# Performance work log

Measured on AMD Instinct MI355X. Metric: run time of the kernel, lower is better.

The kernel has to match this reference:

```python
import jax, jax.numpy as jnp
import numpy as np

EPS = 1e-12

def _l2_normalize(v, axis):
    norm = jnp.linalg.norm(v, ord=2, axis=axis, keepdims=True)
    return v / jnp.maximum(norm, EPS)

def setup_inputs() -> dict:
    key = jax.random.key(0)
    k1, k2, k3 = jax.random.split(key, 3)
    B, H, W, D, K = 16, 56, 56, 512, 32
    x = jax.random.normal(k1, (B, H, W, D), dtype=jnp.float32)
    # 1x1 conv weight (no bias): equivalent to a (D,K) matmul; he_normal-ish scale
    Wc = jax.random.normal(k2, (D, K), dtype=jnp.float32) * jnp.sqrt(2.0 / D)
    # cluster centers, original shape (1,1,1,512,32) -> stored as (D,K)
    C = jax.random.normal(k3, (D, K), dtype=jnp.float32) * jnp.sqrt(2.0 / D)
    return {"x": x, "Wc": Wc, "C": C}

def reference(x, Wc, C):
    # soft-assignment: 1x1 conv + softmax over clusters
    s = jnp.einsum('bhwd,dk->bhwk', x, Wc)          # (B,H,W,K)
    a = jax.nn.softmax(s, axis=-1)                   # (B,H,W,K)
    # v[b,d,k] = sum_{h,w} a[b,h,w,k] * (x[b,h,w,d] + C[d,k])
    #          = einsum(a,x) + C * sum_{h,w} a   (avoids (B,H,W,D,K) intermediate)
    ax = jnp.einsum('bhwk,bhwd->bdk', a, x)          # (B,D,K)
    a_sum = jnp.sum(a, axis=(1, 2))                  # (B,K)
    v = ax + C[None, :, :] * a_sum[:, None, :]       # (B,D,K)
    # intra-normalize over cluster axis (dim=2), flatten, L2 normalize
    v = _l2_normalize(v, axis=2)
    v = v.reshape(v.shape[0], -1)                    # (B, D*K)
    return _l2_normalize(v, axis=1)
```

## Files before the change

kernel.cpp:

```cpp
#include <hip/hip_runtime.h>
#include <math.h>


#define BATCH 16
#define HW    3136
#define DIM   512
#define KCL   32
#define NCHK  49
#define SLABF (BATCH * DIM * KCL + 256)

typedef __attribute__((ext_vector_type(8))) short short8;
typedef __attribute__((ext_vector_type(4))) float f32x4;

__device__ __forceinline__ void atomAddF(float* p, float v) {
    unsafeAtomicAdd(p, v);
}

__device__ __forceinline__ unsigned short f2bf(float f) {
    unsigned u = __float_as_uint(f);
    return (unsigned short)((u + 0x7FFFu + ((u >> 16) & 1u)) >> 16);
}

#define XS_STR  136
#define WTC_STR 136
#define AT_STR  72
#define XT_STR  72

#define LOAD_PX(PX, DC)                                                        \
    _Pragma("unroll")                                                          \
    for (int i = 0; i < 8; ++i) {                                              \
        int f = i * 256 + t;                                                   \
        PX[i] = *(const float4*)(x + ((size_t)(n0 + (f >> 5)) * DIM + (DC) + (f & 31) * 4)); \
    }

#define LOAD_WC(WC, DC)                                                        \
    _Pragma("unroll")                                                          \
    for (int i = 0; i < 4; ++i) {                                              \
        int f = i * 256 + t;                                                   \
        WC[i] = *(const float4*)(Wc + (size_t)((DC) + (f >> 3)) * KCL + (f & 7) * 4); \
    }

#define P1_STAGE(PX, WC)                                                       \
    __syncthreads();                                                           \
    _Pragma("unroll")                                                          \
    for (int i = 0; i < 8; ++i) {                                              \
        int f = i * 256 + t;                                                   \
        ushort4 w;                                                             \
        w.x = f2bf(PX[i].x); w.y = f2bf(PX[i].y);                              \
        w.z = f2bf(PX[i].z); w.w = f2bf(PX[i].w);                              \
        *(ushort4*)&xs[(f >> 5) * XS_STR + (f & 31) * 4] = w;                  \
    }                                                                          \
    _Pragma("unroll")                                                          \
    for (int i = 0; i < 4; ++i) {                                              \
        int f  = i * 256 + t;                                                  \
        int d  = f >> 3;                                                       \
        int k4 = (f & 7) * 4;                                                  \
        wt[(k4 + 0) * WTC_STR + d] = f2bf(WC[i].x);                            \
        wt[(k4 + 1) * WTC_STR + d] = f2bf(WC[i].y);                            \
        wt[(k4 + 2) * WTC_STR + d] = f2bf(WC[i].z);                            \
        wt[(k4 + 3) * WTC_STR + d] = f2bf(WC[i].w);                            \
    }                                                                          \
    __syncthreads();

#define P1_MFMA()                                                              \
    _Pragma("unroll")                                                          \
    for (int ds_ = 0; ds_ < 4; ++ds_) {                                        \
        const int dloc = ds_ * 32 + quad * 8;                                  \
        short8 af = *(const short8*)&xs[(wv * 16 + l15) * XS_STR + dloc];      \
        short8 b0 = *(const short8*)&wt[l15 * WTC_STR + dloc];                 \
        short8 b1 = *(const short8*)&wt[(16 + l15) * WTC_STR + dloc];          \
        acc0 = __builtin_amdgcn_mfma_f32_16x16x32_bf16(af, b0, acc0, 0, 0, 0); \
        acc1 = __builtin_amdgcn_mfma_f32_16x16x32_bf16(af, b1, acc1, 0, 0, 0); \
    }

#define LOAD_PF(PF, DC)                                                        \
    _Pragma("unroll")                                                          \
    for (int i = 0; i < 8; ++i) {                                              \
        const int p = (pg0 + 2 * i) * 4;                                       \
        _Pragma("unroll")                                                      \
        for (int j = 0; j < 4; ++j)                                            \
            PF[i * 4 + j] = xb[(size_t)(p + j) * DIM + (DC)];                  \
    }

#define P2_STAGE(PF)                                                           \
    __syncthreads();                                                           \
    _Pragma("unroll")                                                          \
    for (int i = 0; i < 8; ++i) {                                              \
        const int p = (pg0 + 2 * i) * 4;                                       \
        ushort4 w;                                                             \
        w.x = f2bf(PF[i * 4 + 0]); w.y = f2bf(PF[i * 4 + 1]);                  \
        w.z = f2bf(PF[i * 4 + 2]); w.w = f2bf(PF[i * 4 + 3]);                  \
        *(ushort4*)&xs[dl * XT_STR + (p ^ (((dl >> 3) & 7) << 3))] = w;        \
    }                                                                          \
    __syncthreads();

#define P2_MFMA_STORE(DC)                                                      \
    {                                                                          \
        f32x4 z = {0.f, 0.f, 0.f, 0.f};                                        \
        f32x4 pacc[2][2];                                                      \
        pacc[0][0] = z; pacc[0][1] = z; pacc[1][0] = z; pacc[1][1] = z;        \
        _Pragma("unroll")                                                      \
        for (int s_ = 0; s_ < 2; ++s_) {                                       \
            const int pb = s_ * 32 + quad * 8;                                 \
            short8 bf0 = *(const short8*)&aT[l15 * AT_STR + pb];               \
            short8 bf1 = *(const short8*)&aT[(16 + l15) * AT_STR + pb];        \
            _Pragma("unroll")                                                  \
            for (int m2 = 0; m2 < 2; ++m2) {                                   \
                const int dloc = (wv * 2 + m2) * 16 + l15;                     \
                short8 af = *(const short8*)&xs[dloc * XT_STR + (pb ^ (((dloc >> 3) & 7) << 3))]; \
                pacc[m2][0] = __builtin_amdgcn_mfma_f32_16x16x32_bf16(af, bf0, pacc[m2][0], 0, 0, 0); \
                pacc[m2][1] = __builtin_amdgcn_mfma_f32_16x16x32_bf16(af, bf1, pacc[m2][1], 0, 0, 0); \
            }                                                                  \
        }                                                                      \
        _Pragma("unroll")                                                      \
        for (int m2 = 0; m2 < 2; ++m2) {                                       \
            const int dr = (DC) + (wv * 2 + m2) * 16 + quad * 4;               \
            _Pragma("unroll")                                                  \
            for (int r = 0; r < 4; ++r) {                                      \
                vp[(size_t)(dr + r) * KCL + l15]      = pacc[m2][0][r];        \
                vp[(size_t)(dr + r) * KCL + 16 + l15] = pacc[m2][1][r];        \
            }                                                                  \
        }                                                                      \
    }

__global__ __launch_bounds__(256, 3) void k_sax(const float* __restrict__ x,
                                                const float* __restrict__ Wc,
                                                float* __restrict__ vpart,
                                                float* __restrict__ a_sum) {
    __shared__ unsigned short xs[9216];
    __shared__ unsigned short wt[32 * WTC_STR];
    __shared__ unsigned short aT[KCL * AT_STR];
    __shared__ float asum_l[4][32];
    const int t    = threadIdx.x;
    const int lane = t & 63;
    const int wv   = t >> 6;
    const int l15  = lane & 15;
    const int quad = lane >> 4;
    const int n0   = blockIdx.x * 64;
    const int b    = n0 / HW;
    const int ch   = blockIdx.x % NCHK;

    f32x4 acc0 = {0.f, 0.f, 0.f, 0.f};
    f32x4 acc1 = {0.f, 0.f, 0.f, 0.f};

    float4 pxA[8], pxB[8], wcA[4], wcB[4];
    LOAD_PX(pxA, 0);    LOAD_WC(wcA, 0);
    LOAD_PX(pxB, 128);  LOAD_WC(wcB, 128);

    P1_STAGE(pxA, wcA);
    LOAD_PX(pxA, 256);  LOAD_WC(wcA, 256);
    P1_MFMA();
    P1_STAGE(pxB, wcB);
    LOAD_PX(pxB, 384);  LOAD_WC(wcB, 384);
    P1_MFMA();
    P1_STAGE(pxA, wcA);
    P1_MFMA();
    P1_STAGE(pxB, wcB);
    P1_MFMA();

    float at0 = 0.f, at1 = 0.f;
#pragma unroll
    for (int r = 0; r < 4; ++r) {
        float m = fmaxf(acc0[r], acc1[r]);
        m = fmaxf(m, __shfl_xor(m, 1));
        m = fmaxf(m, __shfl_xor(m, 2));
        m = fmaxf(m, __shfl_xor(m, 4));
        m = fmaxf(m, __shfl_xor(m, 8));
        float e0 = __expf(acc0[r] - m);
        float e1 = __expf(acc1[r] - m);
        float s = e0 + e1;
        s += __shfl_xor(s, 1);
        s += __shfl_xor(s, 2);
        s += __shfl_xor(s, 4);
        s += __shfl_xor(s, 8);
        float inv = 1.f / s;
        float a0 = e0 * inv, a1 = e1 * inv;
        const int pos = wv * 16 + quad * 4 + r;
        aT[l15 * AT_STR + pos]        = f2bf(a0);
        aT[(16 + l15) * AT_STR + pos] = f2bf(a1);
        at0 += a0; at1 += a1;
    }
    at0 += __shfl_xor(at0, 16); at0 += __shfl_xor(at0, 32);
    at1 += __shfl_xor(at1, 16); at1 += __shfl_xor(at1, 32);
    if (quad == 0) {
        asum_l[wv][l15]      = at0;
        asum_l[wv][16 + l15] = at1;
    }

    const int dl  = t & 127;
    const int pg0 = t >> 7;
    const float* xb = x + (size_t)n0 * DIM + dl;
    float* vp = vpart + (size_t)ch * SLABF + (size_t)b * DIM * KCL;

    float pfA[32], pfB[32];
    LOAD_PF(pfA, 0);
    LOAD_PF(pfB, 128);

    __syncthreads();
    if (t < 32)
        atomAddF(&a_sum[b * KCL + t],
                 asum_l[0][t] + asum_l[1][t] + asum_l[2][t] + asum_l[3][t]);

    P2_STAGE(pfA);
    LOAD_PF(pfA, 256);
    P2_MFMA_STORE(0);
    P2_STAGE(pfB);
    LOAD_PF(pfB, 384);
    P2_MFMA_STORE(128);
    P2_STAGE(pfA);
    P2_MFMA_STORE(256);
    P2_STAGE(pfB);
    P2_MFMA_STORE(384);
}

__global__ __launch_bounds__(256) void k_norm1(const float* __restrict__ vpart,
                                               const float* __restrict__ a_sum,
                                               const float* __restrict__ Cc,
                                               float* __restrict__ out,
                                               float* __restrict__ ssq) {
    const int t = threadIdx.x;
    const int row = blockIdx.x * 8 + (t >> 5);
    const int k = t & 31;
    const int b = row >> 9;
    const int d = row & 511;

    const float* vp = vpart + (size_t)row * KCL + k;
    float s0 = 0.f, s1 = 0.f, s2 = 0.f, s3 = 0.f;
#pragma unroll
    for (int ps = 0; ps < 48; ps += 4) {
        s0 += vp[(size_t)(ps + 0) * SLABF];
        s1 += vp[(size_t)(ps + 1) * SLABF];
        s2 += vp[(size_t)(ps + 2) * SLABF];
        s3 += vp[(size_t)(ps + 3) * SLABF];
    }
    s0 += vp[(size_t)48 * SLABF];
    float v = (s0 + s1) + (s2 + s3) + Cc[d * KCL + k] * a_sum[b * KCL + k];

    float ss = v * v;
    ss += __shfl_xor(ss, 1, 32);  ss += __shfl_xor(ss, 2, 32);
    ss += __shfl_xor(ss, 4, 32);  ss += __shfl_xor(ss, 8, 32);
    ss += __shfl_xor(ss, 16, 32);
    float inv = 1.f / fmaxf(sqrtf(ss), 1e-12f);
    float r = v * inv;
    out[(size_t)row * KCL + k] = r;

    float bs = r * r;
    for (int off = 32; off > 0; off >>= 1) bs += __shfl_down(bs, off, 64);
    __shared__ float red[4];
    if ((t & 63) == 0) red[t >> 6] = bs;
    __syncthreads();
    if (t == 0) atomAddF(&ssq[b], (red[0] + red[1]) + (red[2] + red[3]));
}

__global__ __launch_bounds__(256) void k_norm2(float* __restrict__ out,
                                               const float* __restrict__ ssq) {
    const int i4 = blockIdx.x * 256 + threadIdx.x;
    const int b = i4 >> 12;
    float inv = 1.f / fmaxf(sqrtf(ssq[b]), 1e-12f);
    float4 v = *(float4*)(out + (size_t)i4 * 4);
    v.x *= inv; v.y *= inv; v.z *= inv; v.w *= inv;
    *(float4*)(out + (size_t)i4 * 4) = v;
}

extern "C" void kernel_launch(void* const* d_in, const int* in_sizes, int n_in,
                              void* d_out, int out_size, void* d_ws, size_t ws_size,
                              hipStream_t stream) {
    const float* x  = (const float*)d_in[0];
    const float* Wc = (const float*)d_in[1];
    const float* Cc = (const float*)d_in[2];
    float* out = (float*)d_out;

    char* ws = (char*)d_ws;
    float* vpart = (float*)ws;
    float* a_sum = (float*)(ws + (size_t)NCHK * SLABF * 4);
    float* ssq   = (float*)(ws + (size_t)NCHK * SLABF * 4 + 2048);

    hipMemsetAsync(a_sum, 0, 2048 + 64, stream);

    k_sax  <<<784, 256, 0, stream>>>(x, Wc, vpart, a_sum);
    k_norm1<<<1024, 256, 0, stream>>>(vpart, a_sum, Cc, out, ssq);
    k_norm2<<<256, 256, 0, stream>>>(out, ssq);
}
```

Baseline: 195.1 us.

## Load phase-1 x fragments directly into registers and stage full Wc once in LDS

Phase 1 of the fused soft-assign kernel no longer stages x tiles through shared memory. Each lane loads its MFMA A-fragment straight from global memory with double-buffered float4 prefetch and converts it to bf16 in registers. The whole Wc matrix is transposed into LDS once at kernel start, and that buffer is reused for the phase-2 x tile. Phase 2 gives each wave its own 32 rows and drops the barrier before each staging step, which removes several barriers and LDS round trips. The risks are higher register pressure and uncoalesced strided row loads, plus possible hazards from the removed barriers.

Result: no change. 198.2 us (+1.6%).

```diff
diff --git a/kernel.cpp b/kernel.cpp
--- a/kernel.cpp
+++ b/kernel.cpp
@@ -21,78 +21,35 @@
     return (unsigned short)((u + 0x7FFFu + ((u >> 16) & 1u)) >> 16);
 }
 
-#define XS_STR  136
-#define WTC_STR 136
-#define AT_STR  72
-#define XT_STR  72
-
-#define LOAD_PX(PX, DC)                                                        \
-    _Pragma("unroll")                                                          \
-    for (int i = 0; i < 8; ++i) {                                              \
-        int f = i * 256 + t;                                                   \
-        PX[i] = *(const float4*)(x + ((size_t)(n0 + (f >> 5)) * DIM + (DC) + (f & 31) * 4)); \
-    }
-
-#define LOAD_WC(WC, DC)                                                        \
-    _Pragma("unroll")                                                          \
-    for (int i = 0; i < 4; ++i) {                                              \
-        int f = i * 256 + t;                                                   \
-        WC[i] = *(const float4*)(Wc + (size_t)((DC) + (f >> 3)) * KCL + (f & 7) * 4); \
-    }
-
-#define P1_STAGE(PX, WC)                                                       \
-    __syncthreads();                                                           \
-    _Pragma("unroll")                                                          \
-    for (int i = 0; i < 8; ++i) {                                              \
-        int f = i * 256 + t;                                                   \
-        ushort4 w;                                                             \
-        w.x = f2bf(PX[i].x); w.y = f2bf(PX[i].y);                              \
-        w.z = f2bf(PX[i].z); w.w = f2bf(PX[i].w);                              \
-        *(ushort4*)&xs[(f >> 5) * XS_STR + (f & 31) * 4] = w;                  \
-    }                                                                          \
-    _Pragma("unroll")                                                          \
-    for (int i = 0; i < 4; ++i) {                                              \
-        int f  = i * 256 + t;                                                  \
-        int d  = f >> 3;                                                       \
-        int k4 = (f & 7) * 4;                                                  \
-        wt[(k4 + 0) * WTC_STR + d] = f2bf(WC[i].x);                            \
-        wt[(k4 + 1) * WTC_STR + d] = f2bf(WC[i].y);                            \
-        wt[(k4 + 2) * WTC_STR + d] = f2bf(WC[i].z);                            \
-        wt[(k4 + 3) * WTC_STR + d] = f2bf(WC[i].w);                            \
-    }                                                                          \
-    __syncthreads();
-
-#define P1_MFMA()                                                              \
-    _Pragma("unroll")                                                          \
-    for (int ds_ = 0; ds_ < 4; ++ds_) {                                        \
-        const int dloc = ds_ * 32 + quad * 8;                                  \
-        short8 af = *(const short8*)&xs[(wv * 16 + l15) * XS_STR + dloc];      \
-        short8 b0 = *(const short8*)&wt[l15 * WTC_STR + dloc];                 \
-        short8 b1 = *(const short8*)&wt[(16 + l15) * WTC_STR + dloc];          \
-        acc0 = __builtin_amdgcn_mfma_f32_16x16x32_bf16(af, b0, acc0, 0, 0, 0); \
-        acc1 = __builtin_amdgcn_mfma_f32_16x16x32_bf16(af, b1, acc1, 0, 0, 0); \
-    }
+__device__ __forceinline__ short8 pack_frag(float4 lo, float4 hi) {
+    union { unsigned short h[8]; short8 s; } r;
+    r.h[0] = f2bf(lo.x); r.h[1] = f2bf(lo.y); r.h[2] = f2bf(lo.z); r.h[3] = f2bf(lo.w);
+    r.h[4] = f2bf(hi.x); r.h[5] = f2bf(hi.y); r.h[6] = f2bf(hi.z); r.h[7] = f2bf(hi.w);
+    return r.s;
+}
+
+#define WT_STR 520
+#define AT_STR 72
+#define XT_STR 72
 
 #define LOAD_PF(PF, DC)                                                        \
     _Pragma("unroll")                                                          \
     for (int i = 0; i < 8; ++i) {                                              \
-        const int p = (pg0 + 2 * i) * 4;                                       \
+        const int p = (ph + 2 * i) * 4;                                        \
         _Pragma("unroll")                                                      \
         for (int j = 0; j < 4; ++j)                                            \
-            PF[i * 4 + j] = xb[(size_t)(p + j) * DIM + (DC)];                  \
+            PF[i * 4 + j] = xc[(size_t)(p + j) * DIM + (DC)];                  \
     }
 
 #define P2_STAGE(PF)                                                           \
-    __syncthreads();                                                           \
     _Pragma("unroll")                                                          \
     for (int i = 0; i < 8; ++i) {                                              \
-        const int p = (pg0 + 2 * i) * 4;                                       \
+        const int p = (ph + 2 * i) * 4;                                        \
         ushort4 w;                                                             \
         w.x = f2bf(PF[i * 4 + 0]); w.y = f2bf(PF[i * 4 + 1]);                  \
         w.z = f2bf(PF[i * 4 + 2]); w.w = f2bf(PF[i * 4 + 3]);                  \
-        *(ushort4*)&xs[dl * XT_STR + (p ^ (((dl >> 3) & 7) << 3))] = w;        \
-    }                                                                          \
-    __syncthreads();
+        *(ushort4*)&xt[xtrow * XT_STR + (p ^ xsw)] = w;                        \
+    }
 
 #define P2_MFMA_STORE(DC)                                                      \
     {                                                                          \
@@ -106,8 +63,8 @@
             short8 bf1 = *(const short8*)&aT[(16 + l15) * AT_STR + pb];        \
             _Pragma("unroll")                                                  \
             for (int m2 = 0; m2 < 2; ++m2) {                                   \
-                const int dloc = (wv * 2 + m2) * 16 + l15;                     \
-                short8 af = *(const short8*)&xs[dloc * XT_STR + (pb ^ (((dloc >> 3) & 7) << 3))]; \
+                const int dloc = wv * 32 + m2 * 16 + l15;                      \
+                short8 af = *(const short8*)&xt[dloc * XT_STR + (pb ^ (((dloc >> 3) & 7) << 3))]; \
                 pacc[m2][0] = __builtin_amdgcn_mfma_f32_16x16x32_bf16(af, bf0, pacc[m2][0], 0, 0, 0); \
                 pacc[m2][1] = __builtin_amdgcn_mfma_f32_16x16x32_bf16(af, bf1, pacc[m2][1], 0, 0, 0); \
             }                                                                  \
@@ -127,9 +84,8 @@
                                                 const float* __restrict__ Wc,
                                                 float* __restrict__ vpart,
                                                 float* __restrict__ a_sum) {
-    __shared__ unsigned short xs[9216];
-    __shared__ unsigned short wt[32 * WTC_STR];
-    __shared__ unsigned short aT[KCL * AT_STR];
+    __shared__ __align__(16) unsigned short wt[32 * WT_STR];
+    __shared__ __align__(16) unsigned short aT[KCL * AT_STR];
     __shared__ float asum_l[4][32];
     const int t    = threadIdx.x;
     const int lane = t & 63;
@@ -140,23 +96,43 @@
     const int b    = n0 / HW;
     const int ch   = blockIdx.x % NCHK;
 
+    const float* xr = x + (size_t)(n0 + wv * 16 + l15) * DIM + quad * 8;
+
+    float4 afb[2][2];
+#pragma unroll
+    for (int c = 0; c < 2; ++c) {
+        afb[c][0] = *(const float4*)(xr + c * 32);
+        afb[c][1] = *(const float4*)(xr + c * 32 + 4);
+    }
+
+#pragma unroll
+    for (int i = 0; i < 16; ++i) {
+        int f  = i * 256 + t;
+        int d  = f >> 3;
+        int k4 = (f & 7) * 4;
+        float4 v = *(const float4*)(Wc + (size_t)d * KCL + k4);
+        wt[(k4 + 0) * WT_STR + d] = f2bf(v.x);
+        wt[(k4 + 1) * WT_STR + d] = f2bf(v.y);
+        wt[(k4 + 2) * WT_STR + d] = f2bf(v.z);
+        wt[(k4 + 3) * WT_STR + d] = f2bf(v.w);
+    }
+    __syncthreads();
+
     f32x4 acc0 = {0.f, 0.f, 0.f, 0.f};
     f32x4 acc1 = {0.f, 0.f, 0.f, 0.f};
-
-    float4 pxA[8], pxB[8], wcA[4], wcB[4];
-    LOAD_PX(pxA, 0);    LOAD_WC(wcA, 0);
-    LOAD_PX(pxB, 128);  LOAD_WC(wcB, 128);
-
-    P1_STAGE(pxA, wcA);
-    LOAD_PX(pxA, 256);  LOAD_WC(wcA, 256);
-    P1_MFMA();
-    P1_STAGE(pxB, wcB);
-    LOAD_PX(pxB, 384);  LOAD_WC(wcB, 384);
-    P1_MFMA();
-    P1_STAGE(pxA, wcA);
-    P1_MFMA();
-    P1_STAGE(pxB, wcB);
-    P1_MFMA();
+#pragma unroll
+    for (int c = 0; c < 16; ++c) {
+        float4 lo = afb[c & 1][0], hi = afb[c & 1][1];
+        if (c < 14) {
+            afb[c & 1][0] = *(const float4*)(xr + (c + 2) * 32);
+            afb[c & 1][1] = *(const float4*)(xr + (c + 2) * 32 + 4);
+        }
+        short8 af = pack_frag(lo, hi);
+        short8 b0 = *(const short8*)&wt[l15 * WT_STR + c * 32 + quad * 8];
+        short8 b1 = *(const short8*)&wt[(16 + l15) * WT_STR + c * 32 + quad * 8];
+        acc0 = __builtin_amdgcn_mfma_f32_16x16x32_bf16(af, b0, acc0, 0, 0, 0);
+        acc1 = __builtin_amdgcn_mfma_f32_16x16x32_bf16(af, b1, acc1, 0, 0, 0);
+    }
 
     float at0 = 0.f, at1 = 0.f;
 #pragma unroll
@@ -187,29 +163,37 @@
         asum_l[wv][16 + l15] = at1;
     }
 
-    const int dl  = t & 127;
-    const int pg0 = t >> 7;
-    const float* xb = x + (size_t)n0 * DIM + dl;
+    const int rw    = lane & 31;
+    const int ph    = lane >> 5;
+    const int xtrow = wv * 32 + rw;
+    const int xsw   = ((xtrow >> 3) & 7) << 3;
+    unsigned short* xt = wt;
+    const float* xc = x + (size_t)n0 * DIM + xtrow;
     float* vp = vpart + (size_t)ch * SLABF + (size_t)b * DIM * KCL;
 
     float pfA[32], pfB[32];
     LOAD_PF(pfA, 0);
-    LOAD_PF(pfB, 128);
 
     __syncthreads();
     if (t < 32)
         atomAddF(&a_sum[b * KCL + t],
                  asum_l[0][t] + asum_l[1][t] + asum_l[2][t] + asum_l[3][t]);
 
+    LOAD_PF(pfB, 128);
+
     P2_STAGE(pfA);
+    __syncthreads();
     LOAD_PF(pfA, 256);
     P2_MFMA_STORE(0);
     P2_STAGE(pfB);
+    __syncthreads();
     LOAD_PF(pfB, 384);
     P2_MFMA_STORE(128);
     P2_STAGE(pfA);
+    __syncthreads();
     P2_MFMA_STORE(256);
     P2_STAGE(pfB);
+    __syncthreads();
     P2_MFMA_STORE(384);
 }
 
```
